# Kernel optimization log

Hardware: AMD Instinct MI355X
Metric: run time of the kernel (lower is better)

The kernel has to match this reference:

```python
import jax, jax.numpy as jnp
import numpy as np

N_NODES = 100000
N_GRAPHS = 64
NEG_SLOPE = 0.1


def lrelu(x):
    return jnp.where(x > 0, x, NEG_SLOPE * x)


def gcn_layer(x, W, b, src, dst, deg_inv_sqrt):
    # PyG GCNConv: x' = D^-1/2 (A + I) D^-1/2 (x W) + b
    h = x @ W  # [N, out]
    norm = (deg_inv_sqrt[src] * deg_inv_sqrt[dst])[:, None]  # [E, 1]
    agg = jax.ops.segment_sum(h[src] * norm, dst, num_segments=N_NODES)
    agg = agg + h * (deg_inv_sqrt ** 2)[:, None]  # self-loop contribution
    return agg + b


def setup_inputs() -> dict:
    key = jax.random.key(0)
    ks = jax.random.split(key, 12)
    E = 1600000
    x = jax.random.normal(ks[0], (N_NODES, 128), dtype=jnp.float32)
    edge_index = jax.random.randint(ks[1], (2, E), 0, N_NODES, dtype=jnp.int32)
    batch = jnp.sort(jax.random.randint(ks[2], (N_NODES,), 0, N_GRAPHS, dtype=jnp.int32))

    def glorot(k, shape):
        fan_in, fan_out = shape
        s = jnp.sqrt(6.0 / (fan_in + fan_out))
        return jax.random.uniform(k, shape, jnp.float32, -s, s)

    return {
        "x": x,
        "edge_index": edge_index,
        "batch": batch,
        "W1": glorot(ks[3], (128, 32)),
        "b1": jnp.zeros((32,), jnp.float32),
        "W2": glorot(ks[4], (32, 64)),
        "b2": jnp.zeros((64,), jnp.float32),
        "Wl1": glorot(ks[5], (64, 128)),
        "bl1": jnp.zeros((128,), jnp.float32),
        "Wl2": glorot(ks[6], (128, 64)),
        "bl2": jnp.zeros((64,), jnp.float32),
        "Wl3": glorot(ks[7], (64, 1)),
        "bl3": jnp.zeros((1,), jnp.float32),
    }


def reference(x, edge_index, batch, W1, b1, W2, b2, Wl1, bl1, Wl2, bl2, Wl3, bl3):
    src, dst = edge_index[0], edge_index[1]
    # degree with self-loops (symmetric norm, all edge weights = 1)
    deg = jax.ops.segment_sum(jnp.ones_like(src, dtype=x.dtype), dst, num_segments=N_NODES) + 1.0
    deg_inv_sqrt = jax.lax.rsqrt(deg)

    h = lrelu(gcn_layer(x, W1, b1, src, dst, deg_inv_sqrt))
    h = gcn_layer(h, W2, b2, src, dst, deg_inv_sqrt)
    g = jax.ops.segment_max(h, batch, num_segments=N_GRAPHS)  # global max pool [G, 64]
    g = lrelu(g @ Wl1 + bl1)
    g = lrelu(g @ Wl2 + bl2)
    return g @ Wl3 + bl3  # [G, 1]
```

## Files before the change

kernel.cpp:

```cpp
#include <hip/hip_runtime.h>
#include <hip/hip_fp16.h>
#include <math.h>

#define N_NODES 100000
#define N_EDGES 1600000
#define N_GRAPHS 64
#define NB 391
#define CAP 5504

__device__ __forceinline__ unsigned f2o(float f) {
    unsigned u = __float_as_uint(f);
    return (u & 0x80000000u) ? ~u : (u | 0x80000000u);
}
__device__ __forceinline__ float o2f(unsigned u) {
    return (u & 0x80000000u) ? __uint_as_float(u & 0x7fffffffu) : __uint_as_float(~u);
}

__device__ __forceinline__ float4 cvt8(float2 raw) {
    __half2 h0 = ((const __half2*)&raw)[0];
    __half2 h1 = ((const __half2*)&raw)[1];
    float2 f0 = __half22float2(h0);
    float2 f1 = __half22float2(h1);
    return make_float4(f0.x, f0.y, f1.x, f1.y);
}
__device__ __forceinline__ float4 loadh8(const __half* p) {
    return cvt8(*(const float2*)p);
}
__device__ __forceinline__ void storeh8(__half* p, float4 v) {
    __half2 o0 = __floats2half2_rn(v.x, v.y);
    __half2 o1 = __floats2half2_rn(v.z, v.w);
    float2 ow;
    ((__half2*)&ow)[0] = o0;
    ((__half2*)&ow)[1] = o1;
    *(float2*)p = ow;
}

typedef _Float16 h2r __attribute__((ext_vector_type(2)));
typedef _Float16 h4  __attribute__((ext_vector_type(4)));
union HB { float4 f4; h2r h[4]; };
union H4 { float2 f2; h4 h; };

__global__ __launch_bounds__(256) void bucket_kernel(const int* __restrict__ src, const int* __restrict__ dst,
                                                     int* __restrict__ bucketCursor, unsigned* __restrict__ ebuf) {
    __shared__ int hist[NB];
    __shared__ int cur[NB];
    int tid = threadIdx.x;
    for (int b = tid; b < NB; b += 256) hist[b] = 0;
    __syncthreads();
    int e0 = blockIdx.x * 3200;
    for (int i = tid; i < 3200; i += 256) {
        int d = dst[e0 + i];
        atomicAdd(&hist[d >> 8], 1);
    }
    __syncthreads();
    for (int b = tid; b < NB; b += 256) {
        int h = hist[b];
        cur[b] = h ? atomicAdd(&bucketCursor[b], h) : 0;
    }
    __syncthreads();
    for (int i = tid; i < 3200; i += 256) {
        int d = dst[e0 + i];
        int s = src[e0 + i];
        int bu = d >> 8;
        int pos = atomicAdd(&cur[bu], 1);
        if (pos < CAP)
            ebuf[(size_t)bu * CAP + pos] = ((unsigned)(d & 255) << 24) | (unsigned)s;
    }
}

__global__ __launch_bounds__(256) void csr_kernel(const unsigned* __restrict__ ebuf,
                                                  const int* __restrict__ bucketCursor,
                                                  int* __restrict__ colb, int* __restrict__ rowptr,
                                                  int* __restrict__ cnt, float* __restrict__ dis) {
    __shared__ unsigned stage[CAP];
    __shared__ int c256[256], row256[256], cur256[256];
    int b = blockIdx.x;
    int tid = threadIdx.x;
    int M = bucketCursor[b];
    if (M > CAP) M = CAP;
    c256[tid] = 0;
    __syncthreads();
    const unsigned* eb = ebuf + (size_t)b * CAP;
    for (int i = tid; i < M; i += 256) atomicAdd(&c256[eb[i] >> 24], 1);
    __syncthreads();
    if (tid < 64) {
        int c0 = c256[tid * 4], c1 = c256[tid * 4 + 1], c2 = c256[tid * 4 + 2], c3 = c256[tid * 4 + 3];
        int s = c0 + c1 + c2 + c3;
        int inc = s;
        #pragma unroll
        for (int o = 1; o < 64; o <<= 1) {
            int v = __shfl_up(inc, o, 64);
            if (tid >= o) inc += v;
        }
        int ex = inc - s;
        row256[tid * 4] = ex;
        row256[tid * 4 + 1] = ex + c0;
        row256[tid * 4 + 2] = ex + c0 + c1;
        row256[tid * 4 + 3] = ex + c0 + c1 + c2;
    }
    __syncthreads();
    cur256[tid] = row256[tid];
    int node = (b << 8) + tid;
    if (node < N_NODES) {
        int c = c256[tid];
        cnt[node] = c;
        dis[node] = rsqrtf((float)(c + 1));
        rowptr[node] = b * CAP + row256[tid];
    }
    __syncthreads();
    for (int i = tid; i < M; i += 256) {
        unsigned p = eb[i];
        int slot = atomicAdd(&cur256[p >> 24], 1);
        stage[slot] = p & 0xFFFFFFu;
    }
    __syncthreads();
    for (int i = tid; i < M; i += 256) colb[b * CAP + i] = (int)stage[i];
}

__global__ __launch_bounds__(256) void gemm1_kernel(const float* __restrict__ x, const float* __restrict__ W1,
                                                    const float* __restrict__ dis, __half* __restrict__ hs1h) {
    __shared__ __half xsh[128][136];
    __shared__ __half wth[32][136];
    int tid = threadIdx.x;
    int r0 = blockIdx.x * 128;
    for (int idx = tid; idx < 128 * 32; idx += 256) {
        int k = idx >> 5, j = idx & 31;
        wth[j][k] = __float2half_rn(W1[idx]);
    }
    for (int idx = tid; idx < 128 * 32; idx += 256) {
        int r = idx >> 5, c4 = idx & 31;
        int gr = r0 + r;
        float4 v = (gr < N_NODES) ? ((const float4*)x)[(size_t)gr * 32 + c4] : make_float4(0.f, 0.f, 0.f, 0.f);
        __half* p = &xsh[r][c4 * 4];
        *(__half2*)p       = __floats2half2_rn(v.x, v.y);
        *(__half2*)(p + 2) = __floats2half2_rn(v.z, v.w);
    }
    __syncthreads();
    int jg = tid & 7;
    int rg = tid >> 3;
    float acc[4][4];
    #pragma unroll
    for (int i = 0; i < 4; i++)
        #pragma unroll
        for (int j = 0; j < 4; j++) acc[i][j] = 0.f;
    for (int kc = 0; kc < 128; kc += 8) {
        HB xr[4], wr[4];
        #pragma unroll
        for (int ri = 0; ri < 4; ri++) xr[ri].f4 = *(const float4*)&xsh[rg + 32 * ri][kc];
        #pragma unroll
        for (int jj = 0; jj < 4; jj++) wr[jj].f4 = *(const float4*)&wth[jg * 4 + jj][kc];
        #pragma unroll
        for (int ri = 0; ri < 4; ri++) {
            #pragma unroll
            for (int jj = 0; jj < 4; jj++) {
                #pragma unroll
                for (int t = 0; t < 4; t++) {
#if defined(__has_builtin) && __has_builtin(__builtin_amdgcn_fdot2)
                    acc[ri][jj] = __builtin_amdgcn_fdot2(xr[ri].h[t], wr[jj].h[t], acc[ri][jj], false);
#else
                    acc[ri][jj] += (float)xr[ri].h[t][0] * (float)wr[jj].h[t][0]
                                 + (float)xr[ri].h[t][1] * (float)wr[jj].h[t][1];
#endif
                }
            }
        }
    }
    #pragma unroll
    for (int ri = 0; ri < 4; ri++) {
        int gr = r0 + rg + 32 * ri;
        if (gr < N_NODES) {
            float dr = dis[gr];
            float2 ow;
            ((__half2*)&ow)[0] = __floats2half2_rn(dr * acc[ri][0], dr * acc[ri][1]);
            ((__half2*)&ow)[1] = __floats2half2_rn(dr * acc[ri][2], dr * acc[ri][3]);
            *(float2*)&hs1h[(size_t)gr * 32 + jg * 4] = ow;
        }
    }
}

__global__ __launch_bounds__(256) void agg1_kernel(const __half* __restrict__ hs1h, const int* __restrict__ colb,
                                                   const int* __restrict__ rowptr, const int* __restrict__ cnt,
                                                   const float* __restrict__ dis, const float* __restrict__ b1,
                                                   __half* __restrict__ t1h) {
    int tid = threadIdx.x;
    int wid = tid >> 6;
    int lane = tid & 63;
    int half = lane >> 5;
    int es = (lane >> 3) & 3;
    int q = lane & 7;
    int w = blockIdx.x * 4 + wid;
    int r0 = w * 4;

    H4 z; z.f2 = make_float2(0.f, 0.f);
    int r = r0 + half;
    int st = rowptr[r];
    int n = cnt[r];
    H4 pS = z, p0 = z, p1 = z, p2 = z, p3 = z, p4 = z, p5 = z;
    if (es == 0) pS.f2 = *(const float2*)(hs1h + (size_t)r * 32 + q * 4);
    {
        int e0 = es, e1 = 4 + es, e2 = 8 + es, e3 = 12 + es, e4 = 16 + es, e5 = 20 + es;
        if (e0 < n) p0.f2 = *(const float2*)(hs1h + (size_t)colb[st + e0] * 32 + q * 4);
        if (e1 < n) p1.f2 = *(const float2*)(hs1h + (size_t)colb[st + e1] * 32 + q * 4);
        if (e2 < n) p2.f2 = *(const float2*)(hs1h + (size_t)colb[st + e2] * 32 + q * 4);
        if (e3 < n) p3.f2 = *(const float2*)(hs1h + (size_t)colb[st + e3] * 32 + q * 4);
        if (e4 < n) p4.f2 = *(const float2*)(hs1h + (size_t)colb[st + e4] * 32 + q * 4);
        if (e5 < n) p5.f2 = *(const float2*)(hs1h + (size_t)colb[st + e5] * 32 + q * 4);
    }
    #pragma unroll
    for (int i = 0; i < 2; i++) {
        int rA = r;
        int stA = st, nA = n;
        H4 rS = pS, v0 = p0, v1 = p1, v2 = p2, v3 = p3, v4 = p4, v5 = p5;
        pS = z; p0 = z; p1 = z; p2 = z; p3 = z; p4 = z; p5 = z;
        if (i == 0) {
            r = r0 + 2 + half;
            st = rowptr[r];
            n = cnt[r];
            if (es == 0) pS.f2 = *(const float2*)(hs1h + (size_t)r * 32 + q * 4);
            int e0 = es, e1 = 4 + es, e2 = 8 + es, e3 = 12 + es, e4 = 16 + es, e5 = 20 + es;
            if (e0 < n) p0.f2 = *(const float2*)(hs1h + (size_t)colb[st + e0] * 32 + q * 4);
            if (e1 < n) p1.f2 = *(const float2*)(hs1h + (size_t)colb[st + e1] * 32 + q * 4);
            if (e2 < n) p2.f2 = *(const float2*)(hs1h + (size_t)colb[st + e2] * 32 + q * 4);
            if (e3 < n) p3.f2 = *(const float2*)(hs1h + (size_t)colb[st + e3] * 32 + q * 4);
            if (e4 < n) p4.f2 = *(const float2*)(hs1h + (size_t)colb[st + e4] * 32 + q * 4);
            if (e5 < n) p5.f2 = *(const float2*)(hs1h + (size_t)colb[st + e5] * 32 + q * 4);
        }
        h4 sh = (rS.h + (v0.h + v1.h)) + ((v2.h + v3.h) + (v4.h + v5.h));
        float4 a = make_float4((float)sh.x, (float)sh.y, (float)sh.z, (float)sh.w);
        for (int k = 24; k < nA; k += 8) {
            int e0 = k + es, e1 = k + 4 + es;
            if (e0 < nA) {
                float4 v = loadh8(hs1h + (size_t)colb[stA + e0] * 32 + q * 4);
                a.x += v.x; a.y += v.y; a.z += v.z; a.w += v.w;
            }
            if (e1 < nA) {
                float4 v = loadh8(hs1h + (size_t)colb[stA + e1] * 32 + q * 4);
                a.x += v.x; a.y += v.y; a.z += v.z; a.w += v.w;
            }
        }
        #pragma unroll
        for (int m = 8; m <= 16; m <<= 1) {
            a.x += __shfl_xor(a.x, m, 64);
            a.y += __shfl_xor(a.y, m, 64);
            a.z += __shfl_xor(a.z, m, 64);
            a.w += __shfl_xor(a.w, m, 64);
        }
        if (es == 0) {
            float4 bv = *(const float4*)&b1[q * 4];
            float dr = dis[rA];
            float4 v;
            v.x = dr * a.x + bv.x; v.y = dr * a.y + bv.y; v.z = dr * a.z + bv.z; v.w = dr * a.w + bv.w;
            v.x = v.x > 0.f ? v.x : 0.1f * v.x;
            v.y = v.y > 0.f ? v.y : 0.1f * v.y;
            v.z = v.z > 0.f ? v.z : 0.1f * v.z;
            v.w = v.w > 0.f ? v.w : 0.1f * v.w;
            v.x *= dr; v.y *= dr; v.z *= dr; v.w *= dr;
            storeh8(t1h + (size_t)rA * 32 + q * 4, v);
        }
    }
}

__global__ __launch_bounds__(256) void agg2_kernel(const __half* __restrict__ t1h, const int* __restrict__ colb,
                                                   const int* __restrict__ rowptr, const int* __restrict__ cnt,
                                                   const float* __restrict__ dis,
                                                   float* __restrict__ agg32) {
    int tid = threadIdx.x;
    int wid = tid >> 6;
    int lane = tid & 63;
    int half = lane >> 5;
    int es = (lane >> 3) & 3;
    int q = lane & 7;
    int w = blockIdx.x * 4 + wid;
    int r0 = w * 4;

    H4 z; z.f2 = make_float2(0.f, 0.f);
    int r = r0 + half;
    int st = rowptr[r];
    int n = cnt[r];
    H4 pS = z, p0 = z, p1 = z, p2 = z, p3 = z, p4 = z, p5 = z;
    if (es == 0) pS.f2 = *(const float2*)(t1h + (size_t)r * 32 + q * 4);
    {
        int e0 = es, e1 = 4 + es, e2 = 8 + es, e3 = 12 + es, e4 = 16 + es, e5 = 20 + es;
        if (e0 < n) p0.f2 = *(const float2*)(t1h + (size_t)colb[st + e0] * 32 + q * 4);
        if (e1 < n) p1.f2 = *(const float2*)(t1h + (size_t)colb[st + e1] * 32 + q * 4);
        if (e2 < n) p2.f2 = *(const float2*)(t1h + (size_t)colb[st + e2] * 32 + q * 4);
        if (e3 < n) p3.f2 = *(const float2*)(t1h + (size_t)colb[st + e3] * 32 + q * 4);
        if (e4 < n) p4.f2 = *(const float2*)(t1h + (size_t)colb[st + e4] * 32 + q * 4);
        if (e5 < n) p5.f2 = *(const float2*)(t1h + (size_t)colb[st + e5] * 32 + q * 4);
    }
    #pragma unroll
    for (int i = 0; i < 2; i++) {
        int rA = r;
        int stA = st, nA = n;
        H4 rS = pS, v0 = p0, v1 = p1, v2 = p2, v3 = p3, v4 = p4, v5 = p5;
        pS = z; p0 = z; p1 = z; p2 = z; p3 = z; p4 = z; p5 = z;
        if (i == 0) {
            r = r0 + 2 + half;
            st = rowptr[r];
            n = cnt[r];
            if (es == 0) pS.f2 = *(const float2*)(t1h + (size_t)r * 32 + q * 4);
            int e0 = es, e1 = 4 + es, e2 = 8 + es, e3 = 12 + es, e4 = 16 + es, e5 = 20 + es;
            if (e0 < n) p0.f2 = *(const float2*)(t1h + (size_t)colb[st + e0] * 32 + q * 4);
            if (e1 < n) p1.f2 = *(const float2*)(t1h + (size_t)colb[st + e1] * 32 + q * 4);
            if (e2 < n) p2.f2 = *(const float2*)(t1h + (size_t)colb[st + e2] * 32 + q * 4);
            if (e3 < n) p3.f2 = *(const float2*)(t1h + (size_t)colb[st + e3] * 32 + q * 4);
            if (e4 < n) p4.f2 = *(const float2*)(t1h + (size_t)colb[st + e4] * 32 + q * 4);
            if (e5 < n) p5.f2 = *(const float2*)(t1h + (size_t)colb[st + e5] * 32 + q * 4);
        }
        h4 sh = (rS.h + (v0.h + v1.h)) + ((v2.h + v3.h) + (v4.h + v5.h));
        float4 a = make_float4((float)sh.x, (float)sh.y, (float)sh.z, (float)sh.w);
        for (int k = 24; k < nA; k += 8) {
            int e0 = k + es, e1 = k + 4 + es;
            if (e0 < nA) {
                float4 v = loadh8(t1h + (size_t)colb[stA + e0] * 32 + q * 4);
                a.x += v.x; a.y += v.y; a.z += v.z; a.w += v.w;
            }
            if (e1 < nA) {
                float4 v = loadh8(t1h + (size_t)colb[stA + e1] * 32 + q * 4);
                a.x += v.x; a.y += v.y; a.z += v.z; a.w += v.w;
            }
        }
        #pragma unroll
        for (int m = 8; m <= 16; m <<= 1) {
            a.x += __shfl_xor(a.x, m, 64);
            a.y += __shfl_xor(a.y, m, 64);
            a.z += __shfl_xor(a.z, m, 64);
            a.w += __shfl_xor(a.w, m, 64);
        }
        if (es == 0) {
            float dr = dis[rA];
            float4 o = make_float4(dr * a.x, dr * a.y, dr * a.z, dr * a.w);
            *(float4*)&agg32[(size_t)rA * 32 + q * 4] = o;
        }
    }
}

__global__ __launch_bounds__(256) void gemm2p_kernel(const float* __restrict__ agg32, const float* __restrict__ W2,
                                                     const float* __restrict__ b2, const int* __restrict__ batch,
                                                     unsigned* __restrict__ gbufu) {
    __shared__ float as1[64][32];
    __shared__ float w2s[32][64];
    __shared__ float red[4][64];
    int tid = threadIdx.x;
    int r0 = blockIdx.x * 64;
    for (int idx = tid; idx < 32 * 64; idx += 256) w2s[idx >> 6][idx & 63] = W2[idx];
    for (int idx = tid; idx < 64 * 8; idx += 256) {
        int rl = idx >> 3, qc = idx & 7;
        int gr = r0 + rl;
        float4 v = (gr < N_NODES) ? ((const float4*)agg32)[(size_t)gr * 8 + qc] : make_float4(0.f, 0.f, 0.f, 0.f);
        *(float4*)&as1[rl][qc * 4] = v;
    }
    __syncthreads();
    int j = tid & 63;
    int rq = tid >> 6;
    float w2c[32];
    #pragma unroll
    for (int k = 0; k < 32; k++) w2c[k] = w2s[k][j];
    float bj = b2[j];
    int rend = (r0 + 64 <= N_NODES) ? 64 : (N_NODES - r0);
    int gfirst = batch[r0];
    int glast = batch[r0 + rend - 1];
    bool uni = (gfirst == glast);
    float runmax = -INFINITY;
    for (int i = 0; i < 16; i++) {
        int rl = rq + i * 4;
        if (rl >= rend) break;
        float acc = bj;
        #pragma unroll
        for (int kc = 0; kc < 32; kc += 4) {
            float4 av = *(const float4*)&as1[rl][kc];
            acc += av.x * w2c[kc] + av.y * w2c[kc + 1] + av.z * w2c[kc + 2] + av.w * w2c[kc + 3];
        }
        if (uni) runmax = fmaxf(runmax, acc);
        else atomicMax(&gbufu[batch[r0 + rl] * 64 + j], f2o(acc));
    }
    if (uni) {
        red[rq][j] = runmax;
        __syncthreads();
        if (tid < 64) {
            float m = fmaxf(fmaxf(red[0][tid], red[1][tid]), fmaxf(red[2][tid], red[3][tid]));
            atomicMax(&gbufu[gfirst * 64 + tid], f2o(m));
        }
    }
}

__global__ __launch_bounds__(256) void mlp_kernel(const unsigned* __restrict__ gbufu,
                                                  const float* __restrict__ Wl1, const float* __restrict__ bl1,
                                                  const float* __restrict__ Wl2, const float* __restrict__ bl2,
                                                  const float* __restrict__ Wl3, const float* __restrict__ bl3,
                                                  float* __restrict__ out) {
    __shared__ float A[64][64];
    __shared__ float B[64][128];
    int tid = threadIdx.x;
    for (int idx = tid; idx < 64 * 64; idx += 256) A[idx >> 6][idx & 63] = o2f(gbufu[idx]);
    __syncthreads();
    {
        int j = tid & 127;
        int rg = tid >> 7;
        float wc[64];
        #pragma unroll
        for (int k = 0; k < 64; k++) wc[k] = Wl1[k * 128 + j];
        float bj = bl1[j];
        for (int r = rg; r < 64; r += 2) {
            float acc = bj;
            #pragma unroll
            for (int kc = 0; kc < 64; kc += 4) {
                float4 av = *(const float4*)&A[r][kc];
                acc += av.x * wc[kc] + av.y * wc[kc + 1] + av.z * wc[kc + 2] + av.w * wc[kc + 3];
            }
            B[r][j] = acc > 0.f ? acc : 0.1f * acc;
        }
    }
    __syncthreads();
    {
        int j = tid & 63;
        int rg = tid >> 6;
        float wc[128];
        #pragma unroll
        for (int k = 0; k < 128; k++) wc[k] = Wl2[k * 64 + j];
        float bj = bl2[j];
        for (int r = rg; r < 64; r += 4) {
            float acc = bj;
            #pragma unroll
            for (int kc = 0; kc < 128; kc += 4) {
                float4 bv = *(const float4*)&B[r][kc];
                acc += bv.x * wc[kc] + bv.y * wc[kc + 1] + bv.z * wc[kc + 2] + bv.w * wc[kc + 3];
            }
            A[r][j] = acc > 0.f ? acc : 0.1f * acc;
        }
    }
    __syncthreads();
    if (tid < 64) {
        int r = tid;
        float acc = bl3[0];
        #pragma unroll
        for (int k = 0; k < 64; k++) acc += A[r][k] * Wl3[k];
        out[r] = acc;
    }
}

extern "C" void kernel_launch(void* const* d_in, const int* in_sizes, int n_in,
                              void* d_out, int out_size, void* d_ws, size_t ws_size,
                              hipStream_t stream) {
    (void)in_sizes; (void)n_in; (void)out_size; (void)ws_size;
    const float* x    = (const float*)d_in[0];
    const int*   edge = (const int*)d_in[1];
    const int*   batch= (const int*)d_in[2];
    const float* W1   = (const float*)d_in[3];
    const float* b1   = (const float*)d_in[4];
    const float* W2   = (const float*)d_in[5];
    const float* b2   = (const float*)d_in[6];
    const float* Wl1  = (const float*)d_in[7];
    const float* bl1  = (const float*)d_in[8];
    const float* Wl2  = (const float*)d_in[9];
    const float* bl2  = (const float*)d_in[10];
    const float* Wl3  = (const float*)d_in[11];
    const float* bl3  = (const float*)d_in[12];
    const int* srcp = edge;
    const int* dstp = edge + N_EDGES;

    char* ws = (char*)d_ws;
    int*      bucketCursor = (int*)ws;
    unsigned* gbufu        = (unsigned*)(bucketCursor + NB);
    size_t zeroed = (size_t)(NB + N_GRAPHS * 64) * 4;
    size_t off = (zeroed + 255) & ~(size_t)255;
    auto alloc = [&](size_t bytes) { char* p = ws + off; off = (off + bytes + 255) & ~(size_t)255; return p; };
    float*    dis    = (float*)alloc((size_t)N_NODES * 4);
    int*      cnt    = (int*)alloc((size_t)N_NODES * 4);
    int*      rowptr = (int*)alloc((size_t)N_NODES * 4);
    unsigned* ebuf   = (unsigned*)alloc((size_t)NB * CAP * 4);
    int*      colb   = (int*)alloc((size_t)NB * CAP * 4);
    __half*   hs1h   = (__half*)alloc((size_t)N_NODES * 32 * 2);
    __half*   t1h    = (__half*)alloc((size_t)N_NODES * 32 * 2);
    float*    agg32  = (float*)alloc((size_t)N_NODES * 32 * 4);

    hipMemsetAsync(ws, 0, zeroed, stream);

    bucket_kernel<<<500, 256, 0, stream>>>(srcp, dstp, bucketCursor, ebuf);
    csr_kernel   <<<NB, 256, 0, stream>>>(ebuf, bucketCursor, colb, rowptr, cnt, dis);
    gemm1_kernel <<<(N_NODES + 127) / 128, 256, 0, stream>>>(x, W1, dis, hs1h);
    agg1_kernel  <<<6250, 256, 0, stream>>>(hs1h, colb, rowptr, cnt, dis, b1, t1h);
    agg2_kernel  <<<6250, 256, 0, stream>>>(t1h, colb, rowptr, cnt, dis, agg32);
    gemm2p_kernel<<<(N_NODES + 63) / 64, 256, 0, stream>>>(agg32, W2, b2, batch, gbufu);
    mlp_kernel   <<<1, 256, 0, stream>>>(gbufu, Wl1, bl1, Wl2, bl2, Wl3, bl3, (float*)d_out);
}
```

Measured before the change: 272.9 us.

## Fuse layer-2 aggregation with W2 GEMM and max-pool into one kernel

Merges the agg2 gather kernel with the gemm2p kernel, so each 64-row block aggregates neighbor features directly into shared memory and then applies W2, bias and the per-graph max pool. This removes the fp32 agg32 intermediate buffer's global write and read, plus one kernel launch. In exchange, each wave now processes 16 rows sequentially (8 iterations instead of 2), and the grid drops from 6250 to 1563 blocks, which lowers parallelism for latency-bound gathers.

```diff
diff --git a/kernel.cpp b/kernel.cpp
--- a/kernel.cpp
+++ b/kernel.cpp
@@ -260,25 +260,32 @@
     }
 }
 
-__global__ __launch_bounds__(256) void agg2_kernel(const __half* __restrict__ t1h, const int* __restrict__ colb,
-                                                   const int* __restrict__ rowptr, const int* __restrict__ cnt,
-                                                   const float* __restrict__ dis,
-                                                   float* __restrict__ agg32) {
-    int tid = threadIdx.x;
+__global__ __launch_bounds__(256) void agg2gemm_kernel(const __half* __restrict__ t1h, const int* __restrict__ colb,
+                                                       const int* __restrict__ rowptr, const int* __restrict__ cnt,
+                                                       const float* __restrict__ dis,
+                                                       const float* __restrict__ W2, const float* __restrict__ b2,
+                                                       const int* __restrict__ batch, unsigned* __restrict__ gbufu) {
+    __shared__ float as1[64][32];
+    __shared__ float w2s[32][64];
+    __shared__ float red[4][64];
+    int tid = threadIdx.x;
+    int r0 = blockIdx.x * 64;
+    for (int idx = tid; idx < 32 * 64; idx += 256) w2s[idx >> 6][idx & 63] = W2[idx];
+
     int wid = tid >> 6;
     int lane = tid & 63;
     int half = lane >> 5;
     int es = (lane >> 3) & 3;
     int q = lane & 7;
-    int w = blockIdx.x * 4 + wid;
-    int r0 = w * 4;
+    int base = r0 + wid * 16;
 
     H4 z; z.f2 = make_float2(0.f, 0.f);
-    int r = r0 + half;
-    int st = rowptr[r];
-    int n = cnt[r];
+    int r = base + half;
+    bool vld = r < N_NODES;
+    int st = vld ? rowptr[r] : 0;
+    int n  = vld ? cnt[r] : 0;
     H4 pS = z, p0 = z, p1 = z, p2 = z, p3 = z, p4 = z, p5 = z;
-    if (es == 0) pS.f2 = *(const float2*)(t1h + (size_t)r * 32 + q * 4);
+    if (vld && es == 0) pS.f2 = *(const float2*)(t1h + (size_t)r * 32 + q * 4);
     {
         int e0 = es, e1 = 4 + es, e2 = 8 + es, e3 = 12 + es, e4 = 16 + es, e5 = 20 + es;
         if (e0 < n) p0.f2 = *(const float2*)(t1h + (size_t)colb[st + e0] * 32 + q * 4);
@@ -289,16 +296,19 @@
         if (e5 < n) p5.f2 = *(const float2*)(t1h + (size_t)colb[st + e5] * 32 + q * 4);
     }
     #pragma unroll
-    for (int i = 0; i < 2; i++) {
-        int rA = r;
+    for (int i = 0; i < 8; i++) {
+        int rA = i * 2;
+        int rAg = base + rA + half;
+        bool vA = rAg < N_NODES;
         int stA = st, nA = n;
         H4 rS = pS, v0 = p0, v1 = p1, v2 = p2, v3 = p3, v4 = p4, v5 = p5;
         pS = z; p0 = z; p1 = z; p2 = z; p3 = z; p4 = z; p5 = z;
-        if (i == 0) {
-            r = r0 + 2 + half;
-            st = rowptr[r];
-            n = cnt[r];
-            if (es == 0) pS.f2 = *(const float2*)(t1h + (size_t)r * 32 + q * 4);
+        if (i < 7) {
+            r = base + 2 * (i + 1) + half;
+            vld = r < N_NODES;
+            st = vld ? rowptr[r] : 0;
+            n  = vld ? cnt[r] : 0;
+            if (vld && es == 0) pS.f2 = *(const float2*)(t1h + (size_t)r * 32 + q * 4);
             int e0 = es, e1 = 4 + es, e2 = 8 + es, e3 = 12 + es, e4 = 16 + es, e5 = 20 + es;
             if (e0 < n) p0.f2 = *(const float2*)(t1h + (size_t)colb[st + e0] * 32 + q * 4);
             if (e1 < n) p1.f2 = *(const float2*)(t1h + (size_t)colb[st + e1] * 32 + q * 4);
@@ -327,30 +337,14 @@
             a.z += __shfl_xor(a.z, m, 64);
             a.w += __shfl_xor(a.w, m, 64);
         }
-        if (es == 0) {
-            float dr = dis[rA];
+        if (es == 0 && vA) {
+            float dr = dis[rAg];
             float4 o = make_float4(dr * a.x, dr * a.y, dr * a.z, dr * a.w);
-            *(float4*)&agg32[(size_t)rA * 32 + q * 4] = o;
-        }
-    }
-}
-
-__global__ __launch_bounds__(256) void gemm2p_kernel(const float* __restrict__ agg32, const float* __restrict__ W2,
-                                                     const float* __restrict__ b2, const int* __restrict__ batch,
-                                                     unsigned* __restrict__ gbufu) {
-    __shared__ float as1[64][32];
-    __shared__ float w2s[32][64];
-    __shared__ float red[4][64];
-    int tid = threadIdx.x;
-    int r0 = blockIdx.x * 64;
-    for (int idx = tid; idx < 32 * 64; idx += 256) w2s[idx >> 6][idx & 63] = W2[idx];
-    for (int idx = tid; idx < 64 * 8; idx += 256) {
-        int rl = idx >> 3, qc = idx & 7;
-        int gr = r0 + rl;
-        float4 v = (gr < N_NODES) ? ((const float4*)agg32)[(size_t)gr * 8 + qc] : make_float4(0.f, 0.f, 0.f, 0.f);
-        *(float4*)&as1[rl][qc * 4] = v;
-    }
-    __syncthreads();
+            *(float4*)&as1[wid * 16 + rA + half][q * 4] = o;
+        }
+    }
+    __syncthreads();
+
     int j = tid & 63;
     int rq = tid >> 6;
     float w2c[32];
@@ -472,15 +466,13 @@
     int*      colb   = (int*)alloc((size_t)NB * CAP * 4);
     __half*   hs1h   = (__half*)alloc((size_t)N_NODES * 32 * 2);
     __half*   t1h    = (__half*)alloc((size_t)N_NODES * 32 * 2);
-    float*    agg32  = (float*)alloc((size_t)N_NODES * 32 * 4);
 
     hipMemsetAsync(ws, 0, zeroed, stream);
 
-    bucket_kernel<<<500, 256, 0, stream>>>(srcp, dstp, bucketCursor, ebuf);
-    csr_kernel   <<<NB, 256, 0, stream>>>(ebuf, bucketCursor, colb, rowptr, cnt, dis);
-    gemm1_kernel <<<(N_NODES + 127) / 128, 256, 0, stream>>>(x, W1, dis, hs1h);
-    agg1_kernel  <<<6250, 256, 0, stream>>>(hs1h, colb, rowptr, cnt, dis, b1, t1h);
-    agg2_kernel  <<<6250, 256, 0, stream>>>(t1h, colb, rowptr, cnt, dis, agg32);
-    gemm2p_kernel<<<(N_NODES + 63) / 64, 256, 0, stream>>>(agg32, W2, b2, batch, gbufu);
-    mlp_kernel   <<<1, 256, 0, stream>>>(gbufu, Wl1, bl1, Wl2, bl2, Wl3, bl3, (float*)d_out);
-}
+    bucket_kernel  <<<500, 256, 0, stream>>>(srcp, dstp, bucketCursor, ebuf);
+    csr_kernel     <<<NB, 256, 0, stream>>>(ebuf, bucketCursor, colb, rowptr, cnt, dis);
+    gemm1_kernel   <<<(N_NODES + 127) / 128, 256, 0, stream>>>(x, W1, dis, hs1h);
+    agg1_kernel    <<<6250, 256, 0, stream>>>(hs1h, colb, rowptr, cnt, dis, b1, t1h);
+    agg2gemm_kernel<<<(N_NODES + 63) / 64, 256, 0, stream>>>(t1h, colb, rowptr, cnt, dis, W2, b2, batch, gbufu);
+    mlp_kernel     <<<1, 256, 0, stream>>>(gbufu, Wl1, bl1, Wl2, bl2, Wl3, bl3, (float*)d_out);
+}
```

Result: no change. 268.5 us (-1.6%).
